# Performance work log

Hardware: AMD Instinct MI355X
Metric: run time of the kernel (lower is better)

The kernel has to match this reference:

```python
import jax, jax.numpy as jnp
import numpy as np

N, E, C, L, B = 40000, 640000, 128, 3, 64
EPS = 1e-5


def _layer_norm(h, g, b):
    m = h.mean(-1, keepdims=True)
    v = h.var(-1, keepdims=True)
    return (h - m) / jnp.sqrt(v + EPS) * g + b


def setup_inputs() -> dict:
    key = jax.random.key(0)
    ks = jax.random.split(key, 24)
    s = 0.05
    inp = {
        "x": jax.random.normal(ks[0], (N, C), jnp.float32),
        "edge_index": jax.random.randint(ks[1], (2, E), 0, N, dtype=jnp.int32),
        "batch": jnp.sort(jax.random.randint(ks[2], (N,), 0, B, dtype=jnp.int32)),
        # pre-scaler Linear(in=C -> hidden=C)
        "pre_w": jax.random.normal(ks[3], (C, C), jnp.float32) * s,
        "pre_b": jnp.zeros((C,), jnp.float32),
        # per-layer GCNConv weight/bias
        "conv_w": jax.random.normal(ks[4], (L, C, C), jnp.float32) * s,
        "conv_b": jnp.zeros((L, C), jnp.float32),
        # per-layer post-conv LayerNorm (applied for layers 0..L-2)
        "ln_g": jnp.ones((L, C), jnp.float32),
        "ln_b": jnp.zeros((L, C), jnp.float32),
        # per-layer FFN: lin1, lin2, LayerNorm
        "ffn_w1": jax.random.normal(ks[5], (L, C, C), jnp.float32) * s,
        "ffn_b1": jnp.zeros((L, C), jnp.float32),
        "ffn_w2": jax.random.normal(ks[6], (L, C, C), jnp.float32) * s,
        "ffn_b2": jnp.zeros((L, C), jnp.float32),
        "ffn_ln_g": jnp.ones((L, C), jnp.float32),
        "ffn_ln_b": jnp.zeros((L, C), jnp.float32),
        # classifier MLP: Linear(C,C)+ReLU+Linear(C,1)
        "cls_w1": jax.random.normal(ks[7], (C, C), jnp.float32) * s,
        "cls_b1": jnp.zeros((C,), jnp.float32),
        "cls_w2": jax.random.normal(ks[8], (C, 1), jnp.float32) * s,
        "cls_b2": jnp.zeros((1,), jnp.float32),
    }
    return inp


def reference(x, edge_index, batch, pre_w, pre_b, conv_w, conv_b, ln_g, ln_b,
              ffn_w1, ffn_b1, ffn_w2, ffn_b2, ffn_ln_g, ffn_ln_b,
              cls_w1, cls_b1, cls_w2, cls_b2):
    src, dst = edge_index[0], edge_index[1]
    # GCN symmetric normalization with self-loops: deg counts incoming edges + 1
    deg = jax.ops.segment_sum(jnp.ones((E,), x.dtype), dst, num_segments=N) + 1.0
    inv_sqrt = jax.lax.rsqrt(deg)                      # [N]
    norm_e = inv_sqrt[src] * inv_sqrt[dst]             # [E]
    self_norm = inv_sqrt * inv_sqrt                    # [N], 1/deg for self-loop

    h = x @ pre_w + pre_b                              # pre_scaler

    for i in range(L):
        layer_in = h
        hw = h @ conv_w[i]                             # [N,C]
        msg = hw[src] * norm_e[:, None]                # gather + scale [E,C]
        h = jax.ops.segment_sum(msg, dst, num_segments=N)
        h = h + hw * self_norm[:, None] + conv_b[i]    # self-loop + bias
        if i < L - 1:
            h = _layer_norm(h, ln_g[i], ln_b[i])       # norm
            h = jax.nn.relu(h)                         # act (act_first=False)
            h = h + layer_in                           # residual (dropout=0)
            # FFN: lin2(relu(lin1(h))) + h, then norm
            y = jax.nn.relu(h @ ffn_w1[i] + ffn_b1[i]) @ ffn_w2[i] + ffn_b2[i] + h
            h = _layer_norm(y, ffn_ln_g[i], ffn_ln_b[i])

    # global mean pool per graph
    counts = jax.ops.segment_sum(jnp.ones((N,), h.dtype), batch, num_segments=B)
    g = jax.ops.segment_sum(h, batch, num_segments=B) / jnp.maximum(counts, 1.0)[:, None]

    out = jax.nn.relu(g @ cls_w1 + cls_b1) @ cls_w2 + cls_b2   # [B,1]
    return out
```

## Files before the change

### kernel.cpp

```cpp
#include <hip/hip_runtime.h>
#include <hip/hip_fp16.h>
#include <cstdint>
#include <cstddef>

#define N_NODES 40000
#define N_EDGES 640000
#define CH 128
#define NL 3
#define NB 64
#define LN_EPS 1e-5f
#define TSTRIDE 132
#define GBLK 625
#define FBLK 2500

typedef short short8 __attribute__((ext_vector_type(8)));
typedef float floatx4 __attribute__((ext_vector_type(4)));

__device__ __forceinline__ unsigned short bf16_rne(float f) {
    unsigned int u = __float_as_uint(f);
    unsigned int r = u + 0x7FFF + ((u >> 16) & 1);
    return (unsigned short)(r >> 16);
}

__launch_bounds__(256)
__global__ void degpack_kernel(const int* __restrict__ ei, int* __restrict__ degi,
                               const float* __restrict__ pre_w, const float* __restrict__ conv_w,
                               const float* __restrict__ ffn_w1, const float* __restrict__ ffn_w2,
                               short* __restrict__ wpk) {
    int bid = blockIdx.x;
    if (bid < FBLK) {
        int e = bid * 256 + threadIdx.x;
        atomicAdd(&degi[ei[N_EDGES + e]], 1);
        return;
    }
    int idx = (bid - FBLK) * 256 + threadIdx.x;
    int mat = idx >> 14;
    int e = idx & 16383;
    int k = e >> 7, n = e & 127;
    const float* src;
    switch (mat) {
        case 0: src = pre_w; break;
        case 1: case 2: case 3: src = conv_w + (size_t)(mat - 1) * 16384; break;
        case 4: case 5: src = ffn_w1 + (size_t)(mat - 4) * 16384; break;
        default: src = ffn_w2 + (size_t)(mat - 6) * 16384; break;
    }
    float f = src[e];
    unsigned short h = bf16_rne(f);
    float hf = __uint_as_float((unsigned)h << 16);
    unsigned short l = bf16_rne(f - hf);
    int kk = k >> 5, quad = (k >> 3) & 3, j = k & 7;
    int frag = ((kk * 4 + quad) * 128 + n) * 8 + j;
    wpk[(size_t)mat * 32768 + frag] = (short)h;
    wpk[(size_t)mat * 32768 + 16384 + frag] = (short)l;
}

__global__ void scan1_kernel(const int* __restrict__ degi, int* __restrict__ rowptr,
                             int* __restrict__ bsum, float* __restrict__ isq) {
    __shared__ int s[256];
    int t = threadIdx.x;
    int i = blockIdx.x * 256 + t;
    int v = (i < N_NODES) ? degi[i] : 0;
    if (i < N_NODES) isq[i] = rsqrtf((float)v + 1.0f);
    s[t] = v;
    __syncthreads();
    for (int off = 1; off < 256; off <<= 1) {
        int add = (t >= off) ? s[t - off] : 0;
        __syncthreads();
        s[t] += add;
        __syncthreads();
    }
    if (i < N_NODES) rowptr[i + 1] = s[t];
    if (t == 255) bsum[blockIdx.x] = s[255];
}

__global__ void scan23_kernel(const int* __restrict__ bsum, int* __restrict__ rowptr, int nb) {
    __shared__ int s[256];
    int t = threadIdx.x;
    int v = (t < nb) ? bsum[t] : 0;
    s[t] = v;
    __syncthreads();
    for (int off = 1; off < 256; off <<= 1) {
        int add = (t >= off) ? s[t - off] : 0;
        __syncthreads();
        s[t] += add;
        __syncthreads();
    }
    int bid = blockIdx.x;
    int boff = (bid > 0) ? s[bid - 1] : 0;
    int i = bid * 256 + t;
    if (i < N_NODES) rowptr[i + 1] += boff;
    if (i == 0 && bid == 0) rowptr[0] = 0;
}


__device__ __forceinline__ void split8(const float* av, short8& ahi, short8& alo) {
#pragma unroll
    for (int j = 0; j < 8; ++j) {
        unsigned short hb = bf16_rne(av[j]);
        ahi[j] = (short)hb;
        alo[j] = (short)bf16_rne(av[j] - __uint_as_float((unsigned)hb << 16));
    }
}

__device__ __forceinline__ void bload_mfma2(const short* __restrict__ bh,
                                            short8 ahi0, short8 alo0,
                                            short8 ahi1, short8 alo1,
                                            floatx4* acc0, floatx4* acc1) {
    short8 bhi[8], blo[8];
#pragma unroll
    for (int c = 0; c < 8; ++c) {
        bhi[c] = *(const short8*)(bh + c * 128);
        blo[c] = *(const short8*)(bh + 16384 + c * 128);
    }
#pragma unroll
    for (int c = 0; c < 8; ++c) {
        acc0[c] = __builtin_amdgcn_mfma_f32_16x16x32_bf16(ahi0, bhi[c], acc0[c], 0, 0, 0);
        acc0[c] = __builtin_amdgcn_mfma_f32_16x16x32_bf16(alo0, bhi[c], acc0[c], 0, 0, 0);
        acc0[c] = __builtin_amdgcn_mfma_f32_16x16x32_bf16(ahi0, blo[c], acc0[c], 0, 0, 0);
        acc1[c] = __builtin_amdgcn_mfma_f32_16x16x32_bf16(ahi1, bhi[c], acc1[c], 0, 0, 0);
        acc1[c] = __builtin_amdgcn_mfma_f32_16x16x32_bf16(alo1, bhi[c], acc1[c], 0, 0, 0);
        acc1[c] = __builtin_amdgcn_mfma_f32_16x16x32_bf16(ahi1, blo[c], acc1[c], 0, 0, 0);
    }
}

template <int VARIANT>
__device__ __forceinline__ void gemm_core(int tid, int bid,
                                          const float* __restrict__ A, const short* __restrict__ W1pk,
                                          const float* __restrict__ b1, const short* __restrict__ W2pk,
                                          const float* __restrict__ b2, const float* __restrict__ Res,
                                          const float* __restrict__ gamma, const float* __restrict__ beta,
                                          const short* __restrict__ W3pk,
                                          float* __restrict__ OutG, __half* __restrict__ OutC) {
    __shared__ float tbuf[64 * TSTRIDE];
    const int lane = tid & 63;
    const int wv = tid >> 6;
    const int row0 = bid * 64 + wv * 32;
    const int m = lane & 15;
    const int quad = lane >> 4;

    floatx4 acc[2][8];
#pragma unroll
    for (int t = 0; t < 2; ++t)
#pragma unroll
        for (int c = 0; c < 8; ++c) acc[t][c] = (floatx4){0.f, 0.f, 0.f, 0.f};

    const float* arow0 = A + (size_t)(row0 + m) * CH + quad * 8;
    const float* arow1 = arow0 + (size_t)16 * CH;
    float* trow_w = tbuf + (wv * 32) * TSTRIDE;
    const float* trow0 = tbuf + (wv * 32 + m) * TSTRIDE + quad * 8;
    const float* trow1 = trow0 + 16 * TSTRIDE;
    const int boff = quad * 1024 + m * 8;

#pragma unroll 1
    for (int kk = 0; kk < 4; ++kk) {
        float4 a0 = *(const float4*)(arow0 + kk * 32);
        float4 a1 = *(const float4*)(arow0 + kk * 32 + 4);
        float4 a2 = *(const float4*)(arow1 + kk * 32);
        float4 a3 = *(const float4*)(arow1 + kk * 32 + 4);
        float av0[8] = {a0.x, a0.y, a0.z, a0.w, a1.x, a1.y, a1.z, a1.w};
        float av1[8] = {a2.x, a2.y, a2.z, a2.w, a3.x, a3.y, a3.z, a3.w};
        short8 ahi0, alo0, ahi1, alo1;
        split8(av0, ahi0, alo0);
        split8(av1, ahi1, alo1);
        bload_mfma2(W1pk + kk * 4096 + boff, ahi0, alo0, ahi1, alo1, acc[0], acc[1]);
    }

#pragma unroll
    for (int t = 0; t < 2; ++t)
#pragma unroll
    for (int c = 0; c < 8; ++c) {
        int col = c * 16 + m;
        float bv = b1[col];
#pragma unroll
        for (int r = 0; r < 4; ++r) {
            int lrow = t * 16 + quad * 4 + r;
            float v = acc[t][c][r] + bv;
            if (VARIANT == 1) v = fmaxf(v, 0.f);
            trow_w[lrow * TSTRIDE + col] = v;
            if (VARIANT == 0)
                OutG[(size_t)(row0 + lrow) * CH + col] = v;
        }
        acc[t][c] = (floatx4){0.f, 0.f, 0.f, 0.f};
    }

#pragma unroll 1
    for (int kk = 0; kk < 4; ++kk) {
        float av0[8], av1[8];
#pragma unroll
        for (int j = 0; j < 8; ++j) av0[j] = trow0[kk * 32 + j];
#pragma unroll
        for (int j = 0; j < 8; ++j) av1[j] = trow1[kk * 32 + j];
        short8 ahi0, alo0, ahi1, alo1;
        split8(av0, ahi0, alo0);
        split8(av1, ahi1, alo1);
        bload_mfma2(W2pk + kk * 4096 + boff, ahi0, alo0, ahi1, alo1, acc[0], acc[1]);
    }

    if (VARIANT == 0) {
#pragma unroll
        for (int t = 0; t < 2; ++t)
#pragma unroll
        for (int c = 0; c < 8; ++c) {
            int col = c * 16 + m;
#pragma unroll
            for (int r = 0; r < 4; ++r) {
                int row = row0 + t * 16 + quad * 4 + r;
                OutC[(size_t)row * CH + col] = __float2half(acc[t][c][r]);
            }
        }
        return;
    }

#pragma unroll
    for (int t = 0; t < 2; ++t)
#pragma unroll
    for (int c = 0; c < 8; ++c) {
        int col = c * 16 + m;
        float bv = b2[col];
#pragma unroll
        for (int r = 0; r < 4; ++r)
            acc[t][c][r] += bv + Res[(size_t)(row0 + t * 16 + quad * 4 + r) * CH + col];
    }
#pragma unroll
    for (int t = 0; t < 2; ++t)
#pragma unroll
    for (int r = 0; r < 4; ++r) {
        float s = 0.f, q = 0.f;
#pragma unroll
        for (int c = 0; c < 8; ++c) {
            float v = acc[t][c][r];
            s += v;
            q = fmaf(v, v, q);
        }
#pragma unroll
        for (int msk = 1; msk < 16; msk <<= 1) {
            s += __shfl_xor(s, msk);
            q += __shfl_xor(q, msk);
        }
        float mean = s * (1.f / CH);
        float var = q * (1.f / CH) - mean * mean;
        float rstd = rsqrtf(var + LN_EPS);
        int lrow = t * 16 + quad * 4 + r;
        int row = row0 + lrow;
#pragma unroll
        for (int c = 0; c < 8; ++c) {
            int col = c * 16 + m;
            float y = (acc[t][c][r] - mean) * rstd * gamma[col] + beta[col];
            OutG[(size_t)row * CH + col] = y;
            trow_w[lrow * TSTRIDE + col] = y;
        }
    }
#pragma unroll
    for (int t = 0; t < 2; ++t)
#pragma unroll
    for (int c = 0; c < 8; ++c) acc[t][c] = (floatx4){0.f, 0.f, 0.f, 0.f};

#pragma unroll 1
    for (int kk = 0; kk < 4; ++kk) {
        float av0[8], av1[8];
#pragma unroll
        for (int j = 0; j < 8; ++j) av0[j] = trow0[kk * 32 + j];
#pragma unroll
        for (int j = 0; j < 8; ++j) av1[j] = trow1[kk * 32 + j];
        short8 ahi0, alo0, ahi1, alo1;
        split8(av0, ahi0, alo0);
        split8(av1, ahi1, alo1);
        bload_mfma2(W3pk + kk * 4096 + boff, ahi0, alo0, ahi1, alo1, acc[0], acc[1]);
    }

#pragma unroll
    for (int t = 0; t < 2; ++t)
#pragma unroll
    for (int c = 0; c < 8; ++c) {
        int col = c * 16 + m;
#pragma unroll
        for (int r = 0; r < 4; ++r) {
            int row = row0 + t * 16 + quad * 4 + r;
            OutC[(size_t)row * CH + col] = __float2half(acc[t][c][r]);
        }
    }
}

template <int VARIANT>
__launch_bounds__(128, 2)
__global__ void gemm_fused(const float* __restrict__ A, const short* __restrict__ W1pk,
                           const float* __restrict__ b1, const short* __restrict__ W2pk,
                           const float* __restrict__ b2, const float* __restrict__ Res,
                           const float* __restrict__ gamma, const float* __restrict__ beta,
                           const short* __restrict__ W3pk,
                           float* __restrict__ OutG, __half* __restrict__ OutC) {
    gemm_core<VARIANT>(threadIdx.x, blockIdx.x, A, W1pk, b1, W2pk, b2, Res,
                       gamma, beta, W3pk, OutG, OutC);
}

__launch_bounds__(256, 2)
__global__ void fillgemm0_kernel(const int* __restrict__ ei, const int* __restrict__ rowptr,
                                 int* __restrict__ fill, int* __restrict__ srcs,
                                 const float* __restrict__ A, const short* __restrict__ W1pk,
                                 const float* __restrict__ b1, const short* __restrict__ W2pk,
                                 float* __restrict__ OutG, __half* __restrict__ OutC) {
    int bid = blockIdx.x;
    if (bid < GBLK) {
        if (threadIdx.x >= 128) return;
        gemm_core<0>(threadIdx.x, bid, A, W1pk, b1, W2pk, nullptr, nullptr,
                     nullptr, nullptr, nullptr, OutG, OutC);
        return;
    }
    int e = (bid - GBLK) * 256 + threadIdx.x;
    int s = ei[e];
    int d = ei[N_EDGES + e];
    int pos = atomicAdd(&fill[d], 1);
    srcs[rowptr[d] + pos] = s;
}

template <int FUSED>
__launch_bounds__(256)
__global__ void agg_kernel(const __half* __restrict__ HW, const int* __restrict__ rowptr,
                           const int* __restrict__ srcs, const float* __restrict__ isq,
                           const float* __restrict__ bias, const float* __restrict__ gamma,
                           const float* __restrict__ beta, float* __restrict__ Hres,
                           float* __restrict__ Out) {
    const int lane = threadIdx.x & 63;
    const int node = blockIdx.x * 4 + (threadIdx.x >> 6);
    const int start = rowptr[node];
    const int end = rowptr[node + 1];

    float ax = 0.f, ay = 0.f;
    for (int base = start; base < end; base += 64) {
        int idx = base + lane;
        int clamped = (idx < end) ? idx : (end - 1);
        int sl = srcs[clamped];
        float wl = isq[sl];
        int cnt = end - base;
        if (cnt > 64) cnt = 64;
        int j = 0;
        for (; j + 8 <= cnt; j += 8) {
            int s[8];
            float w[8];
            float2 v[8];
#pragma unroll
            for (int q = 0; q < 8; ++q) {
                s[q] = __shfl(sl, j + q);
                w[q] = __shfl(wl, j + q);
            }
#pragma unroll
            for (int q = 0; q < 8; ++q)
                v[q] = __half22float2(*(const __half2*)(HW + (size_t)s[q] * CH + lane * 2));
#pragma unroll
            for (int q = 0; q < 8; ++q) {
                ax = fmaf(w[q], v[q].x, ax);
                ay = fmaf(w[q], v[q].y, ay);
            }
        }
        for (; j + 4 <= cnt; j += 4) {
            int s0 = __shfl(sl, j), s1 = __shfl(sl, j + 1);
            int s2 = __shfl(sl, j + 2), s3 = __shfl(sl, j + 3);
            float w0 = __shfl(wl, j), w1 = __shfl(wl, j + 1);
            float w2 = __shfl(wl, j + 2), w3 = __shfl(wl, j + 3);
            float2 v0 = __half22float2(*(const __half2*)(HW + (size_t)s0 * CH + lane * 2));
            float2 v1 = __half22float2(*(const __half2*)(HW + (size_t)s1 * CH + lane * 2));
            float2 v2 = __half22float2(*(const __half2*)(HW + (size_t)s2 * CH + lane * 2));
            float2 v3 = __half22float2(*(const __half2*)(HW + (size_t)s3 * CH + lane * 2));
            ax = fmaf(w0, v0.x, ax); ay = fmaf(w0, v0.y, ay);
            ax = fmaf(w1, v1.x, ax); ay = fmaf(w1, v1.y, ay);
            ax = fmaf(w2, v2.x, ax); ay = fmaf(w2, v2.y, ay);
            ax = fmaf(w3, v3.x, ax); ay = fmaf(w3, v3.y, ay);
        }
        for (; j < cnt; ++j) {
            int s = __shfl(sl, j);
            float w = __shfl(wl, j);
            float2 vf = __half22float2(*(const __half2*)(HW + (size_t)s * CH + lane * 2));
            ax = fmaf(w, vf.x, ax);
            ay = fmaf(w, vf.y, ay);
        }
    }
    float d = isq[node];
    const __half2 hv = *(const __half2*)(HW + (size_t)node * CH + lane * 2);
    float2 hf = __half22float2(hv);
    const float2 bb = *(const float2*)(bias + lane * 2);
    float hx = d * ax + d * d * hf.x + bb.x;
    float hy = d * ay + d * d * hf.y + bb.y;

    if (!FUSED) {
        float2 o; o.x = hx; o.y = hy;
        *(float2*)(Out + (size_t)node * CH + lane * 2) = o;
        return;
    }
    float sum = hx + hy;
    float sq = hx * hx + hy * hy;
    for (int msk = 1; msk < 64; msk <<= 1) {
        sum += __shfl_xor(sum, msk);
        sq += __shfl_xor(sq, msk);
    }
    float mean = sum * (1.f / CH);
    float var = sq * (1.f / CH) - mean * mean;
    float rstd = rsqrtf(var + LN_EPS);
    const float2 gg = *(const float2*)(gamma + lane * 2);
    const float2 be = *(const float2*)(beta + lane * 2);
    float y0 = (hx - mean) * rstd * gg.x + be.x;
    float y1 = (hy - mean) * rstd * gg.y + be.y;
    float2* hp = (float2*)(Hres + (size_t)node * CH + lane * 2);
    float2 rr = *hp;
    float2 o;
    o.x = fmaxf(y0, 0.f) + rr.x;
    o.y = fmaxf(y1, 0.f) + rr.y;
    *hp = o;
}

__launch_bounds__(256)
__global__ void pool_kernel(const float* __restrict__ H, const int* __restrict__ batch,
                            float* __restrict__ g, float* __restrict__ cntf) {
    const int lane = threadIdx.x & 63;
    const int w = blockIdx.x * 4 + (threadIdx.x >> 6);
    const int n0 = w * 16;
    float lx = 0.f, ly = 0.f;
    int run = 0;
    int cur = batch[n0];
    for (int t = 0; t < 16; ++t) {
        int n = n0 + t;
        int b = batch[n];
        if (b != cur) {
            atomicAdd(&g[(size_t)cur * CH + lane * 2], lx);
            atomicAdd(&g[(size_t)cur * CH + lane * 2 + 1], ly);
            if (lane == 0) atomicAdd(&cntf[cur], (float)run);
            lx = ly = 0.f; run = 0; cur = b;
        }
        const float2 v = *(const float2*)(H + (size_t)n * CH + lane * 2);
        lx += v.x; ly += v.y; ++run;
    }
    atomicAdd(&g[(size_t)cur * CH + lane * 2], lx);
    atomicAdd(&g[(size_t)cur * CH + lane * 2 + 1], ly);
    if (lane == 0) atomicAdd(&cntf[cur], (float)run);
}

__launch_bounds__(128)
__global__ void cls_kernel(const float* __restrict__ g, const float* __restrict__ cntf,
                           const float* __restrict__ w1, const float* __restrict__ b1,
                           const float* __restrict__ w2, const float* __restrict__ b2,
                           float* __restrict__ out) {
    __shared__ float gm[CH];
    __shared__ float red[2];
    const int b = blockIdx.x;
    const int t = threadIdx.x;
    float inv = 1.f / fmaxf(cntf[b], 1.f);
    gm[t] = g[(size_t)b * CH + t] * inv;
    __syncthreads();
    float acc = b1[t];
    for (int k = 0; k < CH; ++k) acc = fmaf(gm[k], w1[(size_t)k * CH + t], acc);
    float v = fmaxf(acc, 0.f) * w2[t];
    for (int msk = 1; msk < 64; msk <<= 1) v += __shfl_xor(v, msk);
    if ((t & 63) == 0) red[t >> 6] = v;
    __syncthreads();
    if (t == 0) out[b] = red[0] + red[1] + b2[0];
}


extern "C" void kernel_launch(void* const* d_in, const int* in_sizes, int n_in,
                              void* d_out, int out_size, void* d_ws, size_t ws_size,
                              hipStream_t stream) {
    const float* x      = (const float*)d_in[0];
    const int*   ei     = (const int*)d_in[1];
    const int*   batch  = (const int*)d_in[2];
    const float* pre_w  = (const float*)d_in[3];
    const float* pre_b  = (const float*)d_in[4];
    const float* conv_w = (const float*)d_in[5];
    const float* conv_b = (const float*)d_in[6];
    const float* ln_g   = (const float*)d_in[7];
    const float* ln_b   = (const float*)d_in[8];
    const float* ffn_w1 = (const float*)d_in[9];
    const float* ffn_b1 = (const float*)d_in[10];
    const float* ffn_w2 = (const float*)d_in[11];
    const float* ffn_b2 = (const float*)d_in[12];
    const float* fln_g  = (const float*)d_in[13];
    const float* fln_b  = (const float*)d_in[14];
    const float* cls_w1 = (const float*)d_in[15];
    const float* cls_b1 = (const float*)d_in[16];
    const float* cls_w2 = (const float*)d_in[17];
    const float* cls_b2 = (const float*)d_in[18];

    float* H    = (float*)d_ws;
    float* T    = H + (size_t)N_NODES * CH;
    float* R    = T + (size_t)N_NODES * CH;
    __half* HWh = (__half*)R;
    int*   degi = (int*)(R + (size_t)N_NODES * CH);
    int*   fill = degi + N_NODES;
    float* g    = (float*)(fill + N_NODES);
    float* cntf = g + (size_t)NB * CH;
    float* isq  = cntf + NB;
    int*  rowptr = (int*)(isq + N_NODES);
    int*  bsum   = rowptr + N_NODES + 1;
    int*  boff   = bsum + 256;
    int*  srcs   = boff + 256;
    short* wpk   = (short*)(srcs + N_EDGES);

    const int nb_scan = (N_NODES + 255) / 256;

    hipMemsetAsync(degi, 0, (size_t)(2 * N_NODES + NB * CH + NB) * sizeof(int), stream);

    degpack_kernel<<<FBLK + 512, 256, 0, stream>>>(ei, degi, pre_w, conv_w,
                                                   ffn_w1, ffn_w2, wpk);
    scan1_kernel<<<nb_scan, 256, 0, stream>>>(degi, rowptr, bsum, isq);
    scan23_kernel<<<nb_scan, 256, 0, stream>>>(bsum, rowptr, nb_scan);
    fillgemm0_kernel<<<GBLK + FBLK, 256, 0, stream>>>(ei, rowptr, fill, srcs,
                                                      x, wpk, pre_b,
                                                      wpk + 1 * 32768, H, HWh);

    const int lblk = N_NODES / 4;

    for (int i = 0; i < NL; ++i) {
        if (i < NL - 1) {
            agg_kernel<1><<<lblk, 256, 0, stream>>>(HWh, rowptr, srcs, isq,
                                                    conv_b + (size_t)i * CH,
                                                    ln_g + (size_t)i * CH,
                                                    ln_b + (size_t)i * CH, H, nullptr);
            gemm_fused<1><<<GBLK, 128, 0, stream>>>(H, wpk + (size_t)(4 + i) * 32768,
                                                    ffn_b1 + (size_t)i * CH,
                                                    wpk + (size_t)(6 + i) * 32768,
                                                    ffn_b2 + (size_t)i * CH, H,
                                                    fln_g + (size_t)i * CH,
                                                    fln_b + (size_t)i * CH,
                                                    wpk + (size_t)(2 + i) * 32768,
                                                    H, HWh);
        } else {
            agg_kernel<0><<<lblk, 256, 0, stream>>>(HWh, rowptr, srcs, isq,
                                                    conv_b + (size_t)i * CH,
                                                    nullptr, nullptr, nullptr, T);
        }
    }

    pool_kernel<<<N_NODES / 64, 256, 0, stream>>>(T, batch, g, cntf);
    cls_kernel<<<NB, CH, 0, stream>>>(g, cntf, cls_w1, cls_b1, cls_w2, cls_b2,
                                      (float*)d_out);
}
```

Measured before the change: 336.6 us.

## Split fused GEMM tiles across four waves by column halves

The fused FFN/conv GEMM kernel now runs 256 threads per block instead of 128. Each pair of waves shares a 32-row slab and each wave computes half of the 128 output columns, so per-wave accumulators and B-register loads are halved. The LayerNorm row statistics now go through shared memory, and block barriers are added between stages because rows are split across waves. The goal is more waves in flight to hide latency, at the cost of extra barriers, extra LDS traffic and duplicated A-operand loading and splitting. A redundant split8 call was also left in the second GEMM loop.

```diff
diff --git a/kernel.cpp b/kernel.cpp
--- a/kernel.cpp
+++ b/kernel.cpp
@@ -102,24 +102,25 @@
     }
 }
 
-__device__ __forceinline__ void bload_mfma2(const short* __restrict__ bh,
-                                            short8 ahi0, short8 alo0,
-                                            short8 ahi1, short8 alo1,
-                                            floatx4* acc0, floatx4* acc1) {
-    short8 bhi[8], blo[8];
-#pragma unroll
-    for (int c = 0; c < 8; ++c) {
-        bhi[c] = *(const short8*)(bh + c * 128);
-        blo[c] = *(const short8*)(bh + 16384 + c * 128);
-    }
-#pragma unroll
-    for (int c = 0; c < 8; ++c) {
-        acc0[c] = __builtin_amdgcn_mfma_f32_16x16x32_bf16(ahi0, bhi[c], acc0[c], 0, 0, 0);
-        acc0[c] = __builtin_amdgcn_mfma_f32_16x16x32_bf16(alo0, bhi[c], acc0[c], 0, 0, 0);
-        acc0[c] = __builtin_amdgcn_mfma_f32_16x16x32_bf16(ahi0, blo[c], acc0[c], 0, 0, 0);
-        acc1[c] = __builtin_amdgcn_mfma_f32_16x16x32_bf16(ahi1, bhi[c], acc1[c], 0, 0, 0);
-        acc1[c] = __builtin_amdgcn_mfma_f32_16x16x32_bf16(alo1, bhi[c], acc1[c], 0, 0, 0);
-        acc1[c] = __builtin_amdgcn_mfma_f32_16x16x32_bf16(ahi1, blo[c], acc1[c], 0, 0, 0);
+__device__ __forceinline__ void loadB4(const short* __restrict__ wb, short8* bh, short8* bl) {
+#pragma unroll
+    for (int cc = 0; cc < 4; ++cc) {
+        bh[cc] = *(const short8*)(wb + cc * 128);
+        bl[cc] = *(const short8*)(wb + 16384 + cc * 128);
+    }
+}
+
+__device__ __forceinline__ void mfma24(const short8* bh, const short8* bl,
+                                       short8 ah0, short8 al0, short8 ah1, short8 al1,
+                                       floatx4* acc0, floatx4* acc1) {
+#pragma unroll
+    for (int cc = 0; cc < 4; ++cc) {
+        acc0[cc] = __builtin_amdgcn_mfma_f32_16x16x32_bf16(ah0, bh[cc], acc0[cc], 0, 0, 0);
+        acc0[cc] = __builtin_amdgcn_mfma_f32_16x16x32_bf16(al0, bh[cc], acc0[cc], 0, 0, 0);
+        acc0[cc] = __builtin_amdgcn_mfma_f32_16x16x32_bf16(ah0, bl[cc], acc0[cc], 0, 0, 0);
+        acc1[cc] = __builtin_amdgcn_mfma_f32_16x16x32_bf16(ah1, bh[cc], acc1[cc], 0, 0, 0);
+        acc1[cc] = __builtin_amdgcn_mfma_f32_16x16x32_bf16(al1, bh[cc], acc1[cc], 0, 0, 0);
+        acc1[cc] = __builtin_amdgcn_mfma_f32_16x16x32_bf16(ah1, bl[cc], acc1[cc], 0, 0, 0);
     }
 }
 
@@ -134,22 +135,24 @@
     __shared__ float tbuf[64 * TSTRIDE];
     const int lane = tid & 63;
     const int wv = tid >> 6;
-    const int row0 = bid * 64 + wv * 32;
+    const int rh = wv >> 1;
+    const int ch = wv & 1;
+    const int row0 = bid * 64 + rh * 32;
     const int m = lane & 15;
     const int quad = lane >> 4;
 
-    floatx4 acc[2][8];
+    floatx4 acc[2][4];
 #pragma unroll
     for (int t = 0; t < 2; ++t)
 #pragma unroll
-        for (int c = 0; c < 8; ++c) acc[t][c] = (floatx4){0.f, 0.f, 0.f, 0.f};
+        for (int cc = 0; cc < 4; ++cc) acc[t][cc] = (floatx4){0.f, 0.f, 0.f, 0.f};
 
     const float* arow0 = A + (size_t)(row0 + m) * CH + quad * 8;
     const float* arow1 = arow0 + (size_t)16 * CH;
-    float* trow_w = tbuf + (wv * 32) * TSTRIDE;
-    const float* trow0 = tbuf + (wv * 32 + m) * TSTRIDE + quad * 8;
+    float* trow_w = tbuf + (rh * 32) * TSTRIDE;
+    const float* trow0 = tbuf + (rh * 32 + m) * TSTRIDE + quad * 8;
     const float* trow1 = trow0 + 16 * TSTRIDE;
-    const int boff = quad * 1024 + m * 8;
+    const int boff = quad * 1024 + m * 8 + ch * 512;
 
 #pragma unroll 1
     for (int kk = 0; kk < 4; ++kk) {
@@ -162,26 +165,125 @@
         short8 ahi0, alo0, ahi1, alo1;
         split8(av0, ahi0, alo0);
         split8(av1, ahi1, alo1);
-        bload_mfma2(W1pk + kk * 4096 + boff, ahi0, alo0, ahi1, alo1, acc[0], acc[1]);
-    }
-
-#pragma unroll
-    for (int t = 0; t < 2; ++t)
-#pragma unroll
-    for (int c = 0; c < 8; ++c) {
-        int col = c * 16 + m;
+        short8 bh[4], bl[4];
+        loadB4(W1pk + kk * 4096 + boff, bh, bl);
+        mfma24(bh, bl, ahi0, alo0, ahi1, alo1, acc[0], acc[1]);
+    }
+
+#pragma unroll
+    for (int cc = 0; cc < 4; ++cc) {
+        int col = (ch * 4 + cc) * 16 + m;
         float bv = b1[col];
+#pragma unroll
+        for (int t = 0; t < 2; ++t)
 #pragma unroll
         for (int r = 0; r < 4; ++r) {
             int lrow = t * 16 + quad * 4 + r;
-            float v = acc[t][c][r] + bv;
+            float v = acc[t][cc][r] + bv;
             if (VARIANT == 1) v = fmaxf(v, 0.f);
             trow_w[lrow * TSTRIDE + col] = v;
             if (VARIANT == 0)
                 OutG[(size_t)(row0 + lrow) * CH + col] = v;
         }
-        acc[t][c] = (floatx4){0.f, 0.f, 0.f, 0.f};
-    }
+#pragma unroll
+        for (int t = 0; t < 2; ++t) acc[t][cc] = (floatx4){0.f, 0.f, 0.f, 0.f};
+    }
+    __syncthreads();
+
+#pragma unroll 1
+    for (int kk = 0; kk < 4; ++kk) {
+        float av0[8], av1[8];
+#pragma unroll
+        for (int j = 0; j < 8; ++j) av0[j] = trow0[kk * 32 + j];
+#pragma unroll
+        for (int j = 0; j < 8; ++j) av1[j] = trow1[kk * 32 + j];
+        short8 ahi0, alo0, ahi1, alo1;
+        split8(av0, ahi0, alo0);
+        split8(av1, alo1, alo1);
+        split8(av1, ahi1, alo1);
+        short8 bh[4], bl[4];
+        loadB4(W2pk + kk * 4096 + boff, bh, bl);
+        mfma24(bh, bl, ahi0, alo0, ahi1, alo1, acc[0], acc[1]);
+    }
+
+    if (VARIANT == 0) {
+#pragma unroll
+        for (int cc = 0; cc < 4; ++cc) {
+            int col = (ch * 4 + cc) * 16 + m;
+#pragma unroll
+            for (int t = 0; t < 2; ++t)
+#pragma unroll
+            for (int r = 0; r < 4; ++r) {
+                int row = row0 + t * 16 + quad * 4 + r;
+                OutC[(size_t)row * CH + col] = __float2half(acc[t][cc][r]);
+            }
+        }
+        return;
+    }
+
+#pragma unroll
+    for (int cc = 0; cc < 4; ++cc) {
+        int col = (ch * 4 + cc) * 16 + m;
+        float bv = b2[col];
+#pragma unroll
+        for (int t = 0; t < 2; ++t)
+#pragma unroll
+        for (int r = 0; r < 4; ++r)
+            acc[t][cc][r] += bv + Res[(size_t)(row0 + t * 16 + quad * 4 + r) * CH + col];
+    }
+#pragma unroll
+    for (int cc = 0; cc < 4; ++cc) {
+        int col = (ch * 4 + cc) * 16 + m;
+#pragma unroll
+        for (int t = 0; t < 2; ++t)
+#pragma unroll
+        for (int r = 0; r < 4; ++r)
+            trow_w[(t * 16 + quad * 4 + r) * TSTRIDE + col] = acc[t][cc][r];
+    }
+    __syncthreads();
+    float mn[2][4], rs[2][4];
+#pragma unroll
+    for (int t = 0; t < 2; ++t)
+#pragma unroll
+    for (int r = 0; r < 4; ++r) {
+        const float* rowp = trow_w + (t * 16 + quad * 4 + r) * TSTRIDE;
+        float s = 0.f, q = 0.f;
+#pragma unroll
+        for (int c = 0; c < 8; ++c) {
+            float v = rowp[c * 16 + m];
+            s += v;
+            q = fmaf(v, v, q);
+        }
+#pragma unroll
+        for (int msk = 1; msk < 16; msk <<= 1) {
+            s += __shfl_xor(s, msk);
+            q += __shfl_xor(q, msk);
+        }
+        float mean = s * (1.f / CH);
+        float var = q * (1.f / CH) - mean * mean;
+        mn[t][r] = mean;
+        rs[t][r] = rsqrtf(var + LN_EPS);
+    }
+    __syncthreads();
+#pragma unroll
+    for (int t = 0; t < 2; ++t)
+#pragma unroll
+    for (int r = 0; r < 4; ++r) {
+        int lrow = t * 16 + quad * 4 + r;
+        int row = row0 + lrow;
+#pragma unroll
+        for (int cc = 0; cc < 4; ++cc) {
+            int col = (ch * 4 + cc) * 16 + m;
+            float y = (acc[t][cc][r] - mn[t][r]) * rs[t][r] * gamma[col] + beta[col];
+            OutG[(size_t)row * CH + col] = y;
+            trow_w[lrow * TSTRIDE + col] = y;
+        }
+    }
+#pragma unroll
+    for (int t = 0; t < 2; ++t)
+#pragma unroll
+    for (int cc = 0; cc < 4; ++cc) acc[t][cc] = (floatx4){0.f, 0.f, 0.f, 0.f};
+    __syncthreads();
 
 #pragma unroll 1
     for (int kk = 0; kk < 4; ++kk) {
@@ -193,96 +295,26 @@
         short8 ahi0, alo0, ahi1, alo1;
         split8(av0, ahi0, alo0);
         split8(av1, ahi1, alo1);
-        bload_mfma2(W2pk + kk * 4096 + boff, ahi0, alo0, ahi1, alo1, acc[0], acc[1]);
-    }
-
-    if (VARIANT == 0) {
+        short8 bh[4], bl[4];
+        loadB4(W3pk + kk * 4096 + boff, bh, bl);
+        mfma24(bh, bl, ahi0, alo0, ahi1, alo1, acc[0], acc[1]);
+    }
+
+#pragma unroll
+    for (int cc = 0; cc < 4; ++cc) {
+        int col = (ch * 4 + cc) * 16 + m;
 #pragma unroll
         for (int t = 0; t < 2; ++t)
-#pragma unroll
-        for (int c = 0; c < 8; ++c) {
-            int col = c * 16 + m;
-#pragma unroll
-            for (int r = 0; r < 4; ++r) {
-                int row = row0 + t * 16 + quad * 4 + r;
-                OutC[(size_t)row * CH + col] = __float2half(acc[t][c][r]);
-            }
-        }
-        return;
-    }
-
-#pragma unroll
-    for (int t = 0; t < 2; ++t)
-#pragma unroll
-    for (int c = 0; c < 8; ++c) {
-        int col = c * 16 + m;
-        float bv = b2[col];
-#pragma unroll
-        for (int r = 0; r < 4; ++r)
-            acc[t][c][r] += bv + Res[(size_t)(row0 + t * 16 + quad * 4 + r) * CH + col];
-    }
-#pragma unroll
-    for (int t = 0; t < 2; ++t)
-#pragma unroll
-    for (int r = 0; r < 4; ++r) {
-        float s = 0.f, q = 0.f;
-#pragma unroll
-        for (int c = 0; c < 8; ++c) {
-            float v = acc[t][c][r];
-            s += v;
-            q = fmaf(v, v, q);
-        }
-#pragma unroll
-        for (int msk = 1; msk < 16; msk <<= 1) {
-            s += __shfl_xor(s, msk);
-            q += __shfl_xor(q, msk);
-        }
-        float mean = s * (1.f / CH);
-        float var = q * (1.f / CH) - mean * mean;
-        float rstd = rsqrtf(var + LN_EPS);
-        int lrow = t * 16 + quad * 4 + r;
-        int row = row0 + lrow;
-#pragma unroll
-        for (int c = 0; c < 8; ++c) {
-            int col = c * 16 + m;
-            float y = (acc[t][c][r] - mean) * rstd * gamma[col] + beta[col];
-            OutG[(size_t)row * CH + col] = y;
-            trow_w[lrow * TSTRIDE + col] = y;
-        }
-    }
-#pragma unroll
-    for (int t = 0; t < 2; ++t)
-#pragma unroll
-    for (int c = 0; c < 8; ++c) acc[t][c] = (floatx4){0.f, 0.f, 0.f, 0.f};
-
-#pragma unroll 1
-    for (int kk = 0; kk < 4; ++kk) {
-        float av0[8], av1[8];
-#pragma unroll
-        for (int j = 0; j < 8; ++j) av0[j] = trow0[kk * 32 + j];
-#pragma unroll
-        for (int j = 0; j < 8; ++j) av1[j] = trow1[kk * 32 + j];
-        short8 ahi0, alo0, ahi1, alo1;
-        split8(av0, ahi0, alo0);
-        split8(av1, ahi1, alo1);
-        bload_mfma2(W3pk + kk * 4096 + boff, ahi0, alo0, ahi1, alo1, acc[0], acc[1]);
-    }
-
-#pragma unroll
-    for (int t = 0; t < 2; ++t)
-#pragma unroll
-    for (int c = 0; c < 8; ++c) {
-        int col = c * 16 + m;
 #pragma unroll
         for (int r = 0; r < 4; ++r) {
             int row = row0 + t * 16 + quad * 4 + r;
-            OutC[(size_t)row * CH + col] = __float2half(acc[t][c][r]);
+            OutC[(size_t)row * CH + col] = __float2half(acc[t][cc][r]);
         }
     }
 }
 
 template <int VARIANT>
-__launch_bounds__(128, 2)
+__launch_bounds__(256)
 __global__ void gemm_fused(const float* __restrict__ A, const short* __restrict__ W1pk,
                            const float* __restrict__ b1, const short* __restrict__ W2pk,
                            const float* __restrict__ b2, const float* __restrict__ Res,
@@ -293,7 +325,7 @@
                        gamma, beta, W3pk, OutG, OutC);
 }
 
-__launch_bounds__(256, 2)
+__launch_bounds__(256)
 __global__ void fillgemm0_kernel(const int* __restrict__ ei, const int* __restrict__ rowptr,
                                  int* __restrict__ fill, int* __restrict__ srcs,
                                  const float* __restrict__ A, const short* __restrict__ W1pk,
@@ -301,7 +333,6 @@
                                  float* __restrict__ OutG, __half* __restrict__ OutC) {
     int bid = blockIdx.x;
     if (bid < GBLK) {
-        if (threadIdx.x >= 128) return;
         gemm_core<0>(threadIdx.x, bid, A, W1pk, b1, W2pk, nullptr, nullptr,
                      nullptr, nullptr, nullptr, OutG, OutC);
         return;
@@ -513,7 +544,7 @@
                                                     conv_b + (size_t)i * CH,
                                                     ln_g + (size_t)i * CH,
                                                     ln_b + (size_t)i * CH, H, nullptr);
-            gemm_fused<1><<<GBLK, 128, 0, stream>>>(H, wpk + (size_t)(4 + i) * 32768,
+            gemm_fused<1><<<GBLK, 256, 0, stream>>>(H, wpk + (size_t)(4 + i) * 32768,
                                                     ffn_b1 + (size_t)i * CH,
                                                     wpk + (size_t)(6 + i) * 32768,
                                                     ffn_b2 + (size_t)i * CH, H,
```

Measured after the change: 354.8 us. 1.05x slower.
